# Optimization experiments

Hardware: AMD Instinct MI355X
Metric: run time of the kernel (lower is better)

The kernel has to match this reference:

```python
import jax, jax.numpy as jnp
import numpy as np

B, I, H, V = 256, 512, 1024, 512


def _lstm_cell(x, h, c, W, U, b):
    # Keras LSTMCell: z = x@kernel + h@recurrent_kernel + bias, gate order i,f,g,o
    z = x @ W + h @ U + b  # [B, 4H]
    i, f, g, o = jnp.split(z, 4, axis=-1)
    i = jax.nn.sigmoid(i)
    f = jax.nn.sigmoid(f)
    g = jnp.tanh(g)
    o = jax.nn.sigmoid(o)
    c_new = f * c + i * g
    h_new = o * jnp.tanh(c_new)
    return h_new, c_new


def setup_inputs() -> dict:
    key = jax.random.key(0)
    ks = jax.random.split(key, 16)
    s_in = 1.0 / np.sqrt(I)
    s_h = 1.0 / np.sqrt(H)
    inp = {
        'x': jax.random.normal(ks[0], (B, I), jnp.float32),
        'h0': jax.random.normal(ks[1], (B, H), jnp.float32) * 0.1,
        'c0': jax.random.normal(ks[2], (B, H), jnp.float32) * 0.1,
        'h1': jax.random.normal(ks[3], (B, H), jnp.float32) * 0.1,
        'c1': jax.random.normal(ks[4], (B, H), jnp.float32) * 0.1,
        'h2': jax.random.normal(ks[5], (B, H), jnp.float32) * 0.1,
        'c2': jax.random.normal(ks[6], (B, H), jnp.float32) * 0.1,
        'W0': jax.random.normal(ks[7], (I, 4 * H), jnp.float32) * s_in,
        'U0': jax.random.normal(ks[8], (H, 4 * H), jnp.float32) * s_h,
        'b0': jnp.zeros((4 * H,), jnp.float32),
        'W1': jax.random.normal(ks[9], (H, 4 * H), jnp.float32) * s_h,
        'U1': jax.random.normal(ks[10], (H, 4 * H), jnp.float32) * s_h,
        'b1': jnp.zeros((4 * H,), jnp.float32),
        'W2': jax.random.normal(ks[11], (H, 4 * H), jnp.float32) * s_h,
        'U2': jax.random.normal(ks[12], (H, 4 * H), jnp.float32) * s_h,
        'b2': jnp.zeros((4 * H,), jnp.float32),
        'Wp': jax.random.normal(ks[13], (H, V), jnp.float32) * s_h,
        'bp': jnp.zeros((V,), jnp.float32),
    }
    return inp


def reference(x, h0, c0, h1, c1, h2, c2, W0, U0, b0, W1, U1, b1, W2, U2, b2, Wp, bp):
    # Stacked LSTM cells: output of each cell feeds the next
    h0n, c0n = _lstm_cell(x, h0, c0, W0, U0, b0)
    h1n, c1n = _lstm_cell(h0n, h1, c1, W1, U1, b1)
    h2n, c2n = _lstm_cell(h1n, h2, c2, W2, U2, b2)
    # Dense output projection on final cell output
    step_logits = h2n @ Wp + bp  # [B, V]
    return (step_logits, h0n, c0n, h1n, c1n, h2n, c2n)
```

## Files before the change

kernel.cpp:

```cpp
#include <hip/hip_runtime.h>


typedef __attribute__((ext_vector_type(8))) short short8_t;
typedef __attribute__((ext_vector_type(8))) unsigned short ushort8_t;
typedef __attribute__((ext_vector_type(4))) unsigned short ushort4_t;
typedef __attribute__((ext_vector_type(4))) float f32x4;

__device__ __forceinline__ unsigned short f2bf(float f) {
    union { float f; unsigned u; } v; v.f = f;
    unsigned r = v.u + 0x7FFFu + ((v.u >> 16) & 1u);
    return (unsigned short)(r >> 16);
}

#define KT 64
#define BN 64

__global__ __launch_bounds__(512, 1)
void gemm64(const unsigned short* __restrict__ A1, const float* __restrict__ W1, int K1,
            const unsigned short* __restrict__ A2, const float* __restrict__ W2,
            int N, int Ktot, int lgs, float* __restrict__ zp)
{
    __shared__ unsigned short Al[2][256 * KT];
    __shared__ unsigned short Wl[2][BN * KT];

    const int tid  = threadIdx.x;
    const int lane = tid & 63;
    const int w    = tid >> 6;
    const int lg   = lane >> 4;
    const int lr   = lane & 15;
    const int nsplit = 1 << lgs;
    const int kb   = blockIdx.x & (nsplit - 1);
    const int ns   = blockIdx.x >> lgs;
    const int n0   = ns * BN;
    const int m0   = w * 32;
    const int klen = Ktot >> lgs;
    const int kbeg = kb * klen;
    const int nt   = klen >> 6;

    const int wr = tid >> 3;
    const int wq = tid & 7;

    ushort8_t pa0[4], pa1[4], pa2[4], pa3[4];
    f32x4     pw0[2], pw1[2], pw2[2], pw3[2];

    f32x4 acc[2][4];
#pragma unroll
    for (int i = 0; i < 2; ++i)
#pragma unroll
        for (int j = 0; j < 4; ++j) acc[i][j] = f32x4{0.f, 0.f, 0.f, 0.f};

    auto issue = [&](int t, ushort8_t (&pa)[4], f32x4 (&pw)[2]) {
        int k0 = kbeg + t * KT;
        const unsigned short* A; const float* Wm; int ldA, krel;
        if (k0 < K1) { A = A1; Wm = W1; ldA = K1;        krel = k0; }
        else         { A = A2; Wm = W2; ldA = Ktot - K1; krel = k0 - K1; }
#pragma unroll
        for (int it = 0; it < 4; ++it) {
            int c = tid + it * 512;
            int row = c >> 3, cc = c & 7;
            pa[it] = *(const ushort8_t*)(A + (size_t)row * ldA + krel + cc * 8);
        }
        const float* wrow = Wm + (size_t)(krel + wr) * N + n0;
        pw[0] = *(const f32x4*)(wrow + wq * 4);
        pw[1] = *(const f32x4*)(wrow + (wq + 8) * 4);
    };

    auto stage = [&](ushort8_t (&pa)[4], f32x4 (&pw)[2],
                     unsigned short* al, unsigned short* wl) {
#pragma unroll
        for (int it = 0; it < 4; ++it) {
            int c = tid + it * 512;
            int row = c >> 3, cc = c & 7;
            *(ushort8_t*)(al + row * KT + ((cc ^ (row & 7)) << 3)) = pa[it];
        }
        int kch = wr >> 3, kwi = wr & 7;
#pragma unroll
        for (int p = 0; p < 2; ++p) {
            int qq = wq + p * 8;
#pragma unroll
            for (int j = 0; j < 4; ++j) {
                int n = qq * 4 + j;
                wl[n * KT + ((kch ^ (n & 7)) << 3) + kwi] = f2bf(pw[p][j]);
            }
        }
    };

    auto compute = [&](const unsigned short* al, const unsigned short* wl) {
#pragma unroll
        for (int ks = 0; ks < 2; ++ks) {
            int ch = ks * 4 + lg;
            int r0 = m0 + lr, r1 = r0 + 16;
            short8_t a0 = *(const short8_t*)(al + r0 * KT + ((ch ^ (r0 & 7)) << 3));
            short8_t a1 = *(const short8_t*)(al + r1 * KT + ((ch ^ (r1 & 7)) << 3));
#pragma unroll
            for (int n4 = 0; n4 < 4; ++n4) {
                int nb = n4 * 16 + lr;
                short8_t b = *(const short8_t*)(wl + nb * KT + ((ch ^ (nb & 7)) << 3));
                acc[0][n4] = __builtin_amdgcn_mfma_f32_16x16x32_bf16(a0, b, acc[0][n4], 0, 0, 0);
                acc[1][n4] = __builtin_amdgcn_mfma_f32_16x16x32_bf16(a1, b, acc[1][n4], 0, 0, 0);
            }
        }
    };

    if (0 < nt) issue(0, pa0, pw0);
    if (1 < nt) issue(1, pa1, pw1);
    if (2 < nt) issue(2, pa2, pw2);
    stage(pa0, pw0, Al[0], Wl[0]);
    __syncthreads();

    for (int t = 0; t < nt; t += 4) {
        if (t + 3 < nt) issue(t + 3, pa3, pw3);
        if (t + 1 < nt) stage(pa1, pw1, Al[1], Wl[1]);
        compute(Al[0], Wl[0]);
        __syncthreads();
        if (t + 4 < nt) issue(t + 4, pa0, pw0);
        if (t + 2 < nt) stage(pa2, pw2, Al[0], Wl[0]);
        if (t + 1 < nt) compute(Al[1], Wl[1]);
        __syncthreads();
        if (t + 5 < nt) issue(t + 5, pa1, pw1);
        if (t + 3 < nt) stage(pa3, pw3, Al[1], Wl[1]);
        if (t + 2 < nt) compute(Al[0], Wl[0]);
        __syncthreads();
        if (t + 6 < nt) issue(t + 6, pa2, pw2);
        if (t + 4 < nt) stage(pa0, pw0, Al[0], Wl[0]);
        if (t + 3 < nt) compute(Al[1], Wl[1]);
        __syncthreads();
    }

    float* zq = zp + (size_t)kb * 256 * N;
#pragma unroll
    for (int ms = 0; ms < 2; ++ms)
#pragma unroll
        for (int n4 = 0; n4 < 4; ++n4)
#pragma unroll
            for (int r = 0; r < 4; ++r) {
                int row = m0 + ms * 16 + lg * 4 + r;
                zq[(size_t)row * N + n0 + n4 * 16 + lr] = acc[ms][n4][r];
            }
}

__global__ __launch_bounds__(256)
void lstm_gates(const float* __restrict__ zp, int nsplit,
                const float* __restrict__ bias, const float* __restrict__ c_old,
                float* __restrict__ h_out, float* __restrict__ c_out,
                unsigned short* __restrict__ h_bf)
{
    int t = blockIdx.x * 256 + threadIdx.x;
    int b = t >> 8;
    int n = (t & 255) << 2;
    f32x4 iv = *(const f32x4*)(bias + n);
    f32x4 fv = *(const f32x4*)(bias + 1024 + n);
    f32x4 gv = *(const f32x4*)(bias + 2048 + n);
    f32x4 ov = *(const f32x4*)(bias + 3072 + n);
    for (int kb = 0; kb < nsplit; ++kb) {
        const float* z = zp + (size_t)kb * 1048576 + (size_t)b * 4096;
        iv += *(const f32x4*)(z + n);
        fv += *(const f32x4*)(z + 1024 + n);
        gv += *(const f32x4*)(z + 2048 + n);
        ov += *(const f32x4*)(z + 3072 + n);
    }
    f32x4 cv = *(const f32x4*)(c_old + (size_t)b * 1024 + n);

    f32x4 hn, cn;
    ushort4_t hb;
#pragma unroll
    for (int j = 0; j < 4; ++j) {
        float ii = 1.f / (1.f + __expf(-iv[j]));
        float ff = 1.f / (1.f + __expf(-fv[j]));
        float gg = tanhf(gv[j]);
        float oo = 1.f / (1.f + __expf(-ov[j]));
        float c2 = ff * cv[j] + ii * gg;
        cn[j] = c2;
        float h2 = oo * tanhf(c2);
        hn[j] = h2;
        hb[j] = f2bf(h2);
    }
    *(f32x4*)(c_out + (size_t)b * 1024 + n) = cn;
    *(f32x4*)(h_out + (size_t)b * 1024 + n) = hn;
    *(ushort4_t*)(h_bf + (size_t)b * 1024 + n) = hb;
}

__global__ __launch_bounds__(256)
void finalize_proj(const float* __restrict__ zp, int nsplit,
                   const float* __restrict__ bp, float* __restrict__ logits)
{
    int t = blockIdx.x * 256 + threadIdx.x;
    int i = t * 4;
    f32x4 v = *(const f32x4*)(bp + (i & 511));
    for (int kb = 0; kb < nsplit; ++kb)
        v += *(const f32x4*)(zp + (size_t)kb * 131072 + i);
    *(f32x4*)(logits + i) = v;
}

__global__ __launch_bounds__(256)
void pack_bf16(const float* __restrict__ x,  const float* __restrict__ h0,
               const float* __restrict__ h1, const float* __restrict__ h2,
               unsigned short* __restrict__ xb,  unsigned short* __restrict__ h0b,
               unsigned short* __restrict__ h1b, unsigned short* __restrict__ h2b)
{
    int t = blockIdx.x * 256 + threadIdx.x;
    const float* src; unsigned short* dst; int off;
    if (t < 32768)       { src = x;  dst = xb;  off = t; }
    else if (t < 98304)  { src = h0; dst = h0b; off = t - 32768; }
    else if (t < 163840) { src = h1; dst = h1b; off = t - 98304; }
    else                 { src = h2; dst = h2b; off = t - 163840; }
    f32x4 v = *(const f32x4*)(src + (size_t)off * 4);
    ushort4_t o;
#pragma unroll
    for (int j = 0; j < 4; ++j) o[j] = f2bf(v[j]);
    *(ushort4_t*)(dst + (size_t)off * 4) = o;
}

extern "C" void kernel_launch(void* const* d_in, const int* in_sizes, int n_in,
                              void* d_out, int out_size, void* d_ws, size_t ws_size,
                              hipStream_t stream)
{
    const float* x  = (const float*)d_in[0];
    const float* h0 = (const float*)d_in[1];
    const float* c0 = (const float*)d_in[2];
    const float* h1 = (const float*)d_in[3];
    const float* c1 = (const float*)d_in[4];
    const float* h2 = (const float*)d_in[5];
    const float* c2 = (const float*)d_in[6];
    const float* W0 = (const float*)d_in[7];
    const float* U0 = (const float*)d_in[8];
    const float* b0 = (const float*)d_in[9];
    const float* W1 = (const float*)d_in[10];
    const float* U1 = (const float*)d_in[11];
    const float* b1 = (const float*)d_in[12];
    const float* W2 = (const float*)d_in[13];
    const float* U2 = (const float*)d_in[14];
    const float* b2 = (const float*)d_in[15];
    const float* Wp = (const float*)d_in[16];
    const float* bp = (const float*)d_in[17];

    float* out    = (float*)d_out;
    float* logits = out;
    float* h0n = out + 131072;
    float* c0n = h0n + 262144;
    float* h1n = c0n + 262144;
    float* c1n = h1n + 262144;
    float* h2n = c1n + 262144;
    float* c2n = h2n + 262144;

    const size_t need4 = 16777216ull + 262144ull + 6ull * 524288ull;
    const int nsplit = (ws_size >= need4) ? 4 : 2;
    const int lgs    = (nsplit == 4) ? 2 : 1;
    const size_t zbytes = (size_t)nsplit * 4194304ull;

    char* ws = (char*)d_ws;
    float*          zp   = (float*)ws;
    unsigned short* xb   = (unsigned short*)(ws + zbytes);
    unsigned short* h0b  = (unsigned short*)(ws + zbytes + 262144);
    unsigned short* h1b  = (unsigned short*)(ws + zbytes + 262144 + 524288);
    unsigned short* h2b  = (unsigned short*)(ws + zbytes + 262144 + 2*524288);
    unsigned short* h0nb = (unsigned short*)(ws + zbytes + 262144 + 3*524288);
    unsigned short* h1nb = (unsigned short*)(ws + zbytes + 262144 + 4*524288);
    unsigned short* h2nb = (unsigned short*)(ws + zbytes + 262144 + 5*524288);

    pack_bf16<<<896, 256, 0, stream>>>(x, h0, h1, h2, xb, h0b, h1b, h2b);

    gemm64<<<64 * nsplit, 512, 0, stream>>>(xb, W0, 512, h0b, U0, 4096, 1536, lgs, zp);
    lstm_gates<<<256, 256, 0, stream>>>(zp, nsplit, b0, c0, h0n, c0n, h0nb);

    gemm64<<<64 * nsplit, 512, 0, stream>>>(h0nb, W1, 1024, h1b, U1, 4096, 2048, lgs, zp);
    lstm_gates<<<256, 256, 0, stream>>>(zp, nsplit, b1, c1, h1n, c1n, h1nb);

    gemm64<<<64 * nsplit, 512, 0, stream>>>(h1nb, W2, 1024, h2b, U2, 4096, 2048, lgs, zp);
    lstm_gates<<<256, 256, 0, stream>>>(zp, nsplit, b2, c2, h2n, c2n, h2nb);

    gemm64<<<8 * nsplit, 512, 0, stream>>>(h2nb, Wp, 1024,
                                           (const unsigned short*)nullptr,
                                           (const float*)nullptr, 512, 1024, lgs, zp);
    finalize_proj<<<128, 256, 0, stream>>>(zp, nsplit, bp, logits);
}
```

Measured before the change: 82.22 us.

## Restructure LSTM GEMM to load A fragments directly into registers with smaller tiles

The GEMM kernel no longer stages the activation matrix in shared memory. Each wave loads its A fragments straight from global memory into registers, and only the fp32-to-bf16 converted weight tile goes through LDS. The tile width drops from 64 to 32 columns and M is split into two halves, which gives many more blocks (occupancy hint of 4 per SM). K-split falls from 4 to 2, which cuts partial-sum traffic and reduction work. The trade-off is that A rows are re-read across column strips without LDS sharing, and the pipeline now uses triple register buffering with lighter barriers.

```diff
diff --git a/kernel.cpp b/kernel.cpp
--- a/kernel.cpp
+++ b/kernel.cpp
@@ -2,7 +2,6 @@
 
 
 typedef __attribute__((ext_vector_type(8))) short short8_t;
-typedef __attribute__((ext_vector_type(8))) unsigned short ushort8_t;
 typedef __attribute__((ext_vector_type(4))) unsigned short ushort4_t;
 typedef __attribute__((ext_vector_type(4))) float f32x4;
 
@@ -13,26 +12,32 @@
 }
 
 #define KT 64
-#define BN 64
-
-__global__ __launch_bounds__(512, 1)
-void gemm64(const unsigned short* __restrict__ A1, const float* __restrict__ W1, int K1,
-            const unsigned short* __restrict__ A2, const float* __restrict__ W2,
-            int N, int Ktot, int lgs, float* __restrict__ zp)
-{
-    __shared__ unsigned short Al[2][256 * KT];
-    __shared__ unsigned short Wl[2][BN * KT];
+#define BN 32
+
+__global__ __launch_bounds__(512, 4)
+void gemm_ar(const unsigned short* __restrict__ A1, const float* __restrict__ W1, int K1,
+             const unsigned short* __restrict__ A2, const float* __restrict__ W2,
+             int N, int Ktot, int lgs, int nstrips, float* __restrict__ zp)
+{
+    __shared__ unsigned short Wl0[BN * KT];
+    __shared__ unsigned short Wl1[BN * KT];
 
     const int tid  = threadIdx.x;
     const int lane = tid & 63;
     const int w    = tid >> 6;
+    const int mg   = w >> 1;
+    const int ng   = w & 1;
     const int lg   = lane >> 4;
     const int lr   = lane & 15;
+
     const int nsplit = 1 << lgs;
     const int kb   = blockIdx.x & (nsplit - 1);
-    const int ns   = blockIdx.x >> lgs;
+    const int rest = blockIdx.x >> lgs;
+    const int ns   = rest % nstrips;
+    const int mh   = rest / nstrips;
+
     const int n0   = ns * BN;
-    const int m0   = w * 32;
+    const int m0   = mh * 128 + mg * 32;
     const int klen = Ktot >> lgs;
     const int kbeg = kb * klen;
     const int nt   = klen >> 6;
@@ -40,103 +45,89 @@
     const int wr = tid >> 3;
     const int wq = tid & 7;
 
-    ushort8_t pa0[4], pa1[4], pa2[4], pa3[4];
-    f32x4     pw0[2], pw1[2], pw2[2], pw3[2];
-
-    f32x4 acc[2][4];
-#pragma unroll
-    for (int i = 0; i < 2; ++i)
-#pragma unroll
-        for (int j = 0; j < 4; ++j) acc[i][j] = f32x4{0.f, 0.f, 0.f, 0.f};
-
-    auto issue = [&](int t, ushort8_t (&pa)[4], f32x4 (&pw)[2]) {
+    short8_t a0[4], a1[4], a2[4];
+    f32x4    w0, w1, w2;
+
+    f32x4 acc0 = {0.f,0.f,0.f,0.f}, acc1 = {0.f,0.f,0.f,0.f};
+
+    auto issueA = [&](int t, short8_t (&a)[4]) {
         int k0 = kbeg + t * KT;
-        const unsigned short* A; const float* Wm; int ldA, krel;
-        if (k0 < K1) { A = A1; Wm = W1; ldA = K1;        krel = k0; }
-        else         { A = A2; Wm = W2; ldA = Ktot - K1; krel = k0 - K1; }
-#pragma unroll
-        for (int it = 0; it < 4; ++it) {
-            int c = tid + it * 512;
-            int row = c >> 3, cc = c & 7;
-            pa[it] = *(const ushort8_t*)(A + (size_t)row * ldA + krel + cc * 8);
+        const unsigned short* A; int ldA, krel;
+        if (k0 < K1) { A = A1; ldA = K1;        krel = k0; }
+        else         { A = A2; ldA = Ktot - K1; krel = k0 - K1; }
+        const unsigned short* base = A + (size_t)(m0 + lr) * ldA + krel + lg * 8;
+        a[0] = *(const short8_t*)(base);
+        a[1] = *(const short8_t*)(base + (size_t)16 * ldA);
+        a[2] = *(const short8_t*)(base + 32);
+        a[3] = *(const short8_t*)(base + (size_t)16 * ldA + 32);
+    };
+
+    auto issueW = [&](int t, f32x4& wv) {
+        int k0 = kbeg + t * KT;
+        const float* Wm; int krel;
+        if (k0 < K1) { Wm = W1; krel = k0; }
+        else         { Wm = W2; krel = k0 - K1; }
+        wv = *(const f32x4*)(Wm + (size_t)(krel + wr) * N + n0 + wq * 4);
+    };
+
+    auto stageW = [&](const f32x4& wv, unsigned short* wl) {
+        int kch = wr >> 3, kwi = wr & 7;
+#pragma unroll
+        for (int j = 0; j < 4; ++j) {
+            int n = wq * 4 + j;
+            wl[n * KT + ((kch ^ (n & 7)) << 3) + kwi] = f2bf(wv[j]);
         }
-        const float* wrow = Wm + (size_t)(krel + wr) * N + n0;
-        pw[0] = *(const f32x4*)(wrow + wq * 4);
-        pw[1] = *(const f32x4*)(wrow + (wq + 8) * 4);
-    };
-
-    auto stage = [&](ushort8_t (&pa)[4], f32x4 (&pw)[2],
-                     unsigned short* al, unsigned short* wl) {
-#pragma unroll
-        for (int it = 0; it < 4; ++it) {
-            int c = tid + it * 512;
-            int row = c >> 3, cc = c & 7;
-            *(ushort8_t*)(al + row * KT + ((cc ^ (row & 7)) << 3)) = pa[it];
-        }
-        int kch = wr >> 3, kwi = wr & 7;
-#pragma unroll
-        for (int p = 0; p < 2; ++p) {
-            int qq = wq + p * 8;
-#pragma unroll
-            for (int j = 0; j < 4; ++j) {
-                int n = qq * 4 + j;
-                wl[n * KT + ((kch ^ (n & 7)) << 3) + kwi] = f2bf(pw[p][j]);
-            }
-        }
-    };
-
-    auto compute = [&](const unsigned short* al, const unsigned short* wl) {
+    };
+
+    auto compute = [&](const unsigned short* wl, short8_t (&a)[4]) {
 #pragma unroll
         for (int ks = 0; ks < 2; ++ks) {
             int ch = ks * 4 + lg;
-            int r0 = m0 + lr, r1 = r0 + 16;
-            short8_t a0 = *(const short8_t*)(al + r0 * KT + ((ch ^ (r0 & 7)) << 3));
-            short8_t a1 = *(const short8_t*)(al + r1 * KT + ((ch ^ (r1 & 7)) << 3));
-#pragma unroll
-            for (int n4 = 0; n4 < 4; ++n4) {
-                int nb = n4 * 16 + lr;
-                short8_t b = *(const short8_t*)(wl + nb * KT + ((ch ^ (nb & 7)) << 3));
-                acc[0][n4] = __builtin_amdgcn_mfma_f32_16x16x32_bf16(a0, b, acc[0][n4], 0, 0, 0);
-                acc[1][n4] = __builtin_amdgcn_mfma_f32_16x16x32_bf16(a1, b, acc[1][n4], 0, 0, 0);
-            }
+            int nb = ng * 16 + lr;
+            short8_t b = *(const short8_t*)(wl + nb * KT + ((ch ^ (nb & 7)) << 3));
+            acc0 = __builtin_amdgcn_mfma_f32_16x16x32_bf16(a[ks * 2],     b, acc0, 0, 0, 0);
+            acc1 = __builtin_amdgcn_mfma_f32_16x16x32_bf16(a[ks * 2 + 1], b, acc1, 0, 0, 0);
         }
     };
 
-    if (0 < nt) issue(0, pa0, pw0);
-    if (1 < nt) issue(1, pa1, pw1);
-    if (2 < nt) issue(2, pa2, pw2);
-    stage(pa0, pw0, Al[0], Wl[0]);
-    __syncthreads();
-
-    for (int t = 0; t < nt; t += 4) {
-        if (t + 3 < nt) issue(t + 3, pa3, pw3);
-        if (t + 1 < nt) stage(pa1, pw1, Al[1], Wl[1]);
-        compute(Al[0], Wl[0]);
-        __syncthreads();
-        if (t + 4 < nt) issue(t + 4, pa0, pw0);
-        if (t + 2 < nt) stage(pa2, pw2, Al[0], Wl[0]);
-        if (t + 1 < nt) compute(Al[1], Wl[1]);
-        __syncthreads();
-        if (t + 5 < nt) issue(t + 5, pa1, pw1);
-        if (t + 3 < nt) stage(pa3, pw3, Al[1], Wl[1]);
-        if (t + 2 < nt) compute(Al[0], Wl[0]);
-        __syncthreads();
-        if (t + 6 < nt) issue(t + 6, pa2, pw2);
-        if (t + 4 < nt) stage(pa0, pw0, Al[0], Wl[0]);
-        if (t + 3 < nt) compute(Al[1], Wl[1]);
-        __syncthreads();
-    }
+#define BAR() do { asm volatile("s_waitcnt lgkmcnt(0)" ::: "memory"); \
+                   __builtin_amdgcn_s_barrier(); } while (0)
+
+    issueW(0, w0);
+    if (1 < nt) issueW(1, w1);
+    issueA(0, a0);
+    stageW(w0, Wl0);
+    if (2 < nt) issueW(2, w2);
+    if (1 < nt) issueA(1, a1);
+    BAR();
+
+#define PHASE(p, WST, WLST, WIS, AIS, WLC, ACM) \
+    if ((p) < nt) { \
+        if ((p) + 1 < nt) stageW(WST, WLST); \
+        if ((p) + 3 < nt) issueW((p) + 3, WIS); \
+        if ((p) + 2 < nt) issueA((p) + 2, AIS); \
+        compute(WLC, ACM); \
+        BAR(); \
+    }
+
+    for (int t = 0; t < nt; t += 6) {
+        PHASE(t + 0, w1, Wl1, w0, a2, Wl0, a0)
+        PHASE(t + 1, w2, Wl0, w1, a0, Wl1, a1)
+        PHASE(t + 2, w0, Wl1, w2, a1, Wl0, a2)
+        PHASE(t + 3, w1, Wl0, w0, a2, Wl1, a0)
+        PHASE(t + 4, w2, Wl1, w1, a0, Wl0, a1)
+        PHASE(t + 5, w0, Wl0, w2, a1, Wl1, a2)
+    }
+#undef PHASE
+#undef BAR
 
     float* zq = zp + (size_t)kb * 256 * N;
-#pragma unroll
-    for (int ms = 0; ms < 2; ++ms)
-#pragma unroll
-        for (int n4 = 0; n4 < 4; ++n4)
-#pragma unroll
-            for (int r = 0; r < 4; ++r) {
-                int row = m0 + ms * 16 + lg * 4 + r;
-                zq[(size_t)row * N + n0 + n4 * 16 + lr] = acc[ms][n4][r];
-            }
+    const int nc = n0 + ng * 16 + lr;
+#pragma unroll
+    for (int r = 0; r < 4; ++r) {
+        zq[(size_t)(m0 + lg * 4 + r) * N + nc]      = acc0[r];
+        zq[(size_t)(m0 + 16 + lg * 4 + r) * N + nc] = acc1[r];
+    }
 }
 
 __global__ __launch_bounds__(256)
@@ -243,9 +234,9 @@
     float* h2n = c1n + 262144;
     float* c2n = h2n + 262144;
 
-    const size_t need4 = 16777216ull + 262144ull + 6ull * 524288ull;
-    const int nsplit = (ws_size >= need4) ? 4 : 2;
-    const int lgs    = (nsplit == 4) ? 2 : 1;
+    const size_t need2 = 8388608ull + 262144ull + 6ull * 524288ull;
+    const int nsplit = (ws_size >= need2) ? 2 : 1;
+    const int lgs    = (nsplit == 2) ? 1 : 0;
     const size_t zbytes = (size_t)nsplit * 4194304ull;
 
     char* ws = (char*)d_ws;
@@ -260,17 +251,17 @@
 
     pack_bf16<<<896, 256, 0, stream>>>(x, h0, h1, h2, xb, h0b, h1b, h2b);
 
-    gemm64<<<64 * nsplit, 512, 0, stream>>>(xb, W0, 512, h0b, U0, 4096, 1536, lgs, zp);
+    gemm_ar<<<2 * 128 * nsplit, 512, 0, stream>>>(xb, W0, 512, h0b, U0, 4096, 1536, lgs, 128, zp);
     lstm_gates<<<256, 256, 0, stream>>>(zp, nsplit, b0, c0, h0n, c0n, h0nb);
 
-    gemm64<<<64 * nsplit, 512, 0, stream>>>(h0nb, W1, 1024, h1b, U1, 4096, 2048, lgs, zp);
+    gemm_ar<<<2 * 128 * nsplit, 512, 0, stream>>>(h0nb, W1, 1024, h1b, U1, 4096, 2048, lgs, 128, zp);
     lstm_gates<<<256, 256, 0, stream>>>(zp, nsplit, b1, c1, h1n, c1n, h1nb);
 
-    gemm64<<<64 * nsplit, 512, 0, stream>>>(h1nb, W2, 1024, h2b, U2, 4096, 2048, lgs, zp);
+    gemm_ar<<<2 * 128 * nsplit, 512, 0, stream>>>(h1nb, W2, 1024, h2b, U2, 4096, 2048, lgs, 128, zp);
     lstm_gates<<<256, 256, 0, stream>>>(zp, nsplit, b2, c2, h2n, c2n, h2nb);
 
-    gemm64<<<8 * nsplit, 512, 0, stream>>>(h2nb, Wp, 1024,
-                                           (const unsigned short*)nullptr,
-                                           (const float*)nullptr, 512, 1024, lgs, zp);
+    gemm_ar<<<2 * 16 * nsplit, 512, 0, stream>>>(h2nb, Wp, 1024,
+                                                 (const unsigned short*)nullptr,
+                                                 (const float*)nullptr, 512, 1024, lgs, 16, zp);
     finalize_proj<<<128, 256, 0, stream>>>(zp, nsplit, bp, logits);
 }
```

Result: slower. 128.6 us (+56.4%).
